# Kernel tuning notes

Measured on AMD Instinct MI355X. Metric: run time of the kernel, lower is better.

The kernel has to match this reference:

```python
import jax, jax.numpy as jnp
import numpy as np

N_NODES = 100000
N_EDGES = 3200000
HID = 16


def _graph_conv(x, src, dst, w_rel, w_root, b_rel, num_nodes):
    # PyG GraphConv: out_i = lin_rel(sum_{j in N(i)} x_j) + lin_root(x_i)
    agg = jax.ops.segment_sum(x[src], dst, num_segments=num_nodes)  # [N, d_in]
    return agg @ w_rel + b_rel + x @ w_root


def setup_inputs() -> dict:
    key = jax.random.key(0)
    ks = jax.random.split(key, 8)
    x = jax.random.normal(ks[0], (N_NODES, 1), dtype=jnp.float32)
    edge_index = jax.random.randint(ks[1], (2, N_EDGES), 0, N_NODES, dtype=jnp.int64)
    s = 1.0 / np.sqrt(HID)
    return {
        "x": x,
        "edge_index": edge_index,
        "enc_w_rel": jax.random.uniform(ks[2], (1, HID), jnp.float32, -1.0, 1.0),
        "enc_w_root": jax.random.uniform(ks[3], (1, HID), jnp.float32, -1.0, 1.0),
        "enc_b": jnp.zeros((HID,), jnp.float32),
        "proc_w_rel": jax.random.uniform(ks[4], (HID, HID), jnp.float32, -s, s),
        "proc_w_root": jax.random.uniform(ks[5], (HID, HID), jnp.float32, -s, s),
        "proc_b": jnp.zeros((HID,), jnp.float32),
        "dec_w_rel": jax.random.uniform(ks[6], (HID, 1), jnp.float32, -s, s),
        "dec_w_root": jax.random.uniform(ks[7], (HID, 1), jnp.float32, -s, s),
        "dec_b": jnp.zeros((1,), jnp.float32),
    }


def reference(x, edge_index, enc_w_rel, enc_w_root, enc_b,
              proc_w_rel, proc_w_root, proc_b,
              dec_w_rel, dec_w_root, dec_b):
    num_nodes = x.shape[0]
    src, dst = edge_index[0], edge_index[1]
    z = _graph_conv(x, src, dst, enc_w_rel, enc_w_root, enc_b, num_nodes)
    z = jax.nn.relu(z)
    z = _graph_conv(z, src, dst, proc_w_rel, proc_w_root, proc_b, num_nodes)
    y = _graph_conv(z, src, dst, dec_w_rel, dec_w_root, dec_b, num_nodes)
    return jax.nn.relu(y)
```

## Files before the change

### kernel.cpp

```cpp
#include <hip/hip_runtime.h>

#define HID 16
#define SB_BITS 11
#define SBLK (1 << SB_BITS)
#define NBMAX 64
#define GSTRIDE 16
#define PT_THREADS 512
#define PT_K 8
#define PT_EDGES (PT_THREADS * PT_K)

__global__ void k_init(int* __restrict__ p, int n) {
    int i = blockIdx.x * blockDim.x + threadIdx.x;
    if (i < n) p[i] = 0;
}

__global__ void __launch_bounds__(PT_THREADS)
k_passA(const int* __restrict__ src, const int* __restrict__ dst,
        unsigned* __restrict__ bucketsA, int* __restrict__ gcurA,
        int E, int nb, int capA) {
    __shared__ int cnt[NBMAX];
    __shared__ int pos[NBMAX];
    __shared__ int gbase[NBMAX];
    __shared__ unsigned reorder[PT_EDGES];
    __shared__ unsigned char bbk[PT_EDGES];
    int tb = blockIdx.x * PT_EDGES;
    int nE = min(PT_EDGES, E - tb);
    if (threadIdx.x < nb) cnt[threadIdx.x] = 0;
    __syncthreads();
    int kk[PT_K]; int rk[PT_K]; unsigned pk[PT_K];
    int ebase = tb + threadIdx.x * PT_K;
    if (ebase + PT_K <= E) {
        uint4 s0 = *(const uint4*)(src + ebase);
        uint4 s1 = *(const uint4*)(src + ebase + 4);
        uint4 d0 = *(const uint4*)(dst + ebase);
        uint4 d1 = *(const uint4*)(dst + ebase + 4);
        int ss[PT_K] = {(int)s0.x,(int)s0.y,(int)s0.z,(int)s0.w,
                        (int)s1.x,(int)s1.y,(int)s1.z,(int)s1.w};
        int dd[PT_K] = {(int)d0.x,(int)d0.y,(int)d0.z,(int)d0.w,
                        (int)d1.x,(int)d1.y,(int)d1.z,(int)d1.w};
#pragma unroll
        for (int k = 0; k < PT_K; k++) {
            int b = dd[k] >> SB_BITS;
            kk[k] = b;
            pk[k] = ((unsigned)(dd[k] & (SBLK - 1)) << 17) | (unsigned)ss[k];
            rk[k] = atomicAdd(&cnt[b], 1);
        }
    } else {
#pragma unroll
        for (int k = 0; k < PT_K; k++) {
            int e = ebase + k;
            if (e < E) {
                int s = src[e], d = dst[e];
                int b = d >> SB_BITS;
                kk[k] = b;
                pk[k] = ((unsigned)(d & (SBLK - 1)) << 17) | (unsigned)s;
                rk[k] = atomicAdd(&cnt[b], 1);
            } else kk[k] = -1;
        }
    }
    __syncthreads();
    if (threadIdx.x == 0) {
        int acc = 0;
        for (int b = 0; b < nb; b++) { pos[b] = acc; acc += cnt[b]; }
    }
    __syncthreads();
    if (threadIdx.x < nb && cnt[threadIdx.x] > 0)
        gbase[threadIdx.x] = atomicAdd(&gcurA[threadIdx.x * GSTRIDE], cnt[threadIdx.x]);
    __syncthreads();
#pragma unroll
    for (int k = 0; k < PT_K; k++) {
        if (kk[k] >= 0) {
            int idx = pos[kk[k]] + rk[k];
            reorder[idx] = pk[k];
            bbk[idx] = (unsigned char)kk[k];
        }
    }
    __syncthreads();
    for (int idx = threadIdx.x; idx < nE; idx += PT_THREADS) {
        int b = bbk[idx];
        int g = gbase[b] + (idx - pos[b]);
        if (g < capA) bucketsA[(size_t)b * capA + g] = reorder[idx];
    }
}

__global__ void __launch_bounds__(PT_THREADS)
k_aggA1(const unsigned* __restrict__ bucketsA, const int* __restrict__ gcurA,
        const float* __restrict__ val, float* __restrict__ AGG,
        int capA, int tilesA, int N) {
    int j = blockIdx.x / tilesA;
    int tile = blockIdx.x - j * tilesA;
    int cnt_j = min(gcurA[j * GSTRIDE], capA);
    int tb = tile * PT_EDGES;
    if (tb >= cnt_j) return;
    int nE = min(PT_EDGES, cnt_j - tb);
    __shared__ float acc[SBLK];
    for (int i = threadIdx.x; i < SBLK; i += PT_THREADS) acc[i] = 0.f;
    __syncthreads();
    const unsigned* in = bucketsA + (size_t)j * capA + tb;
    int ebase = threadIdx.x * PT_K;
    if (ebase + PT_K <= nE) {
        uint4 p0 = *(const uint4*)(in + ebase);
        uint4 p1 = *(const uint4*)(in + ebase + 4);
        unsigned pp[PT_K] = {p0.x, p0.y, p0.z, p0.w, p1.x, p1.y, p1.z, p1.w};
        float v[PT_K];
#pragma unroll
        for (int k = 0; k < PT_K; k++) v[k] = val[pp[k] & 0x1FFFFu];
#pragma unroll
        for (int k = 0; k < PT_K; k++) atomicAdd(&acc[pp[k] >> 17], v[k]);
    } else {
#pragma unroll
        for (int k = 0; k < PT_K; k++) {
            int e = ebase + k;
            if (e < nE) {
                unsigned p = in[e];
                atomicAdd(&acc[p >> 17], val[p & 0x1FFFFu]);
            }
        }
    }
    __syncthreads();
    int base_n = j << SB_BITS;
    for (int i = threadIdx.x; i < SBLK; i += PT_THREADS) {
        float v = acc[i];
        int n = base_n + i;
        if (n < N && v != 0.f) atomicAdd(&AGG[n], v);
    }
}

__global__ void __launch_bounds__(PT_THREADS)
k_aggA2(const unsigned* __restrict__ bucketsA, const int* __restrict__ gcurA,
        const float* __restrict__ SAB, float* __restrict__ AGG2,
        int capA, int tilesA, int N) {
    int j = blockIdx.x / tilesA;
    int tile = blockIdx.x - j * tilesA;
    int cnt_j = min(gcurA[j * GSTRIDE], capA);
    int tb = tile * PT_EDGES;
    if (tb >= cnt_j) return;
    int nE = min(PT_EDGES, cnt_j - tb);
    __shared__ float accx[SBLK];
    __shared__ float accy[SBLK];
    for (int i = threadIdx.x; i < SBLK; i += PT_THREADS) { accx[i] = 0.f; accy[i] = 0.f; }
    __syncthreads();
    const unsigned* in = bucketsA + (size_t)j * capA + tb;
    const float2* v2 = (const float2*)SAB;
    int ebase = threadIdx.x * PT_K;
    if (ebase + PT_K <= nE) {
        uint4 p0 = *(const uint4*)(in + ebase);
        uint4 p1 = *(const uint4*)(in + ebase + 4);
        unsigned pp[PT_K] = {p0.x, p0.y, p0.z, p0.w, p1.x, p1.y, p1.z, p1.w};
        float2 v[PT_K];
#pragma unroll
        for (int k = 0; k < PT_K; k++) v[k] = v2[pp[k] & 0x1FFFFu];
#pragma unroll
        for (int k = 0; k < PT_K; k++) {
            int d = (int)(pp[k] >> 17);
            atomicAdd(&accx[d], v[k].x);
            atomicAdd(&accy[d], v[k].y);
        }
    } else {
#pragma unroll
        for (int k = 0; k < PT_K; k++) {
            int e = ebase + k;
            if (e < nE) {
                unsigned p = in[e];
                float2 v = v2[p & 0x1FFFFu];
                int d = (int)(p >> 17);
                atomicAdd(&accx[d], v.x);
                atomicAdd(&accy[d], v.y);
            }
        }
    }
    __syncthreads();
    int base_n = j << SB_BITS;
    for (int i = threadIdx.x; i < SBLK; i += PT_THREADS) {
        float vx = accx[i], vy = accy[i];
        int n = base_n + i;
        if (n < N && (vx != 0.f || vy != 0.f)) {
            atomicAdd(&AGG2[2 * n],     vx);
            atomicAdd(&AGG2[2 * n + 1], vy);
        }
    }
}

__global__ void __launch_bounds__(256)
k_enc(const float* __restrict__ AGG1, const float* __restrict__ x,
      const float* __restrict__ ewrel, const float* __restrict__ ewroot,
      const float* __restrict__ eb,
      const float* __restrict__ pwrel, const float* __restrict__ pwroot,
      const float* __restrict__ dwrel, const float* __restrict__ dwroot,
      float* __restrict__ SAB, float* __restrict__ G1, float* __restrict__ G2,
      int N) {
    __shared__ float su1[HID], su2[HID], sv1[HID], sv2[HID];
    __shared__ float swr[HID], swo[HID], sbb[HID];
    int t = threadIdx.x;
    if (t < 64) {
        int k = t & 15, w = t >> 4;
        const float* M  = (w < 2) ? pwrel : pwroot;
        const float* vv = ((w & 1) == 0) ? dwrel : dwroot;
        float acc = 0.f;
        for (int h = 0; h < HID; h++) acc += M[k * HID + h] * vv[h];
        if (w == 0) su1[k] = acc;
        else if (w == 1) su2[k] = acc;
        else if (w == 2) sv1[k] = acc;
        else sv2[k] = acc;
    }
    if (t < HID) { swr[t] = ewrel[t]; swo[t] = ewroot[t]; sbb[t] = eb[t]; }
    __syncthreads();
    int n = blockIdx.x * 256 + t;
    if (n < N) {
        float a1 = AGG1[n], xi = x[n];
        float sa = 0.f, sb = 0.f, g1 = 0.f, g2 = 0.f;
#pragma unroll
        for (int h = 0; h < HID; h++) {
            float z = fmaxf(fmaf(a1, swr[h], fmaf(xi, swo[h], sbb[h])), 0.f);
            sa = fmaf(z, su1[h], sa);
            sb = fmaf(z, su2[h], sb);
            g1 = fmaf(z, sv1[h], g1);
            g2 = fmaf(z, sv2[h], g2);
        }
        ((float2*)SAB)[n] = make_float2(sa, sb);
        G1[n] = g1; G2[n] = g2;
    }
}

__global__ void __launch_bounds__(256)
k_mid(const float* __restrict__ AGG2, const float* __restrict__ G1,
      const float* __restrict__ G2, const float* __restrict__ pb,
      const float* __restrict__ dwrel, const float* __restrict__ dwroot,
      const float* __restrict__ db,
      float* __restrict__ BETA, float* __restrict__ R, int N) {
    __shared__ float sc1, sc2, sbd;
    if (threadIdx.x == 0) {
        float c1 = 0.f, c2 = 0.f;
        for (int h = 0; h < HID; h++) { c1 += pb[h] * dwrel[h]; c2 += pb[h] * dwroot[h]; }
        sc1 = c1; sc2 = c2; sbd = db[0];
    }
    __syncthreads();
    int n = blockIdx.x * 256 + threadIdx.x;
    if (n < N) {
        float2 a = ((const float2*)AGG2)[n];
        BETA[n] = a.x + G1[n] + sc1;
        R[n]    = a.y + G2[n] + sc2 + sbd;
    }
}

__global__ void __launch_bounds__(256)
k_final(const float* __restrict__ AGG3, const float* __restrict__ R,
        float* __restrict__ out, int N) {
    int n = blockIdx.x * 256 + threadIdx.x;
    if (n < N) out[n] = fmaxf(AGG3[n] + R[n], 0.f);
}

extern "C" void kernel_launch(void* const* d_in, const int* in_sizes, int n_in,
                              void* d_out, int out_size, void* d_ws, size_t ws_size,
                              hipStream_t stream) {
    const float* x      = (const float*)d_in[0];
    const int*   ei     = (const int*)d_in[1];
    const float* ewrel  = (const float*)d_in[2];
    const float* ewroot = (const float*)d_in[3];
    const float* eb     = (const float*)d_in[4];
    const float* pwrel  = (const float*)d_in[5];
    const float* pwroot = (const float*)d_in[6];
    const float* pb     = (const float*)d_in[7];
    const float* dwrel  = (const float*)d_in[8];
    const float* dwroot = (const float*)d_in[9];
    const float* db     = (const float*)d_in[10];
    float* out = (float*)d_out;

    const int N = in_sizes[0];
    const int E = in_sizes[1] / 2;
    const int* src = ei;
    const int* dst = ei + E;

    const int nb = (N + SBLK - 1) >> SB_BITS;
    int capA = ((E / nb + 2048) + PT_EDGES - 1) & ~(PT_EDGES - 1);
    const int tilesA = capA / PT_EDGES;

    size_t off = 0;
    int* gcurA = (int*)d_ws;                    off += NBMAX * GSTRIDE;
    float* AGG1 = (float*)d_ws + off;           off += N;
    float* AGG2 = (float*)d_ws + off;           off += (size_t)2 * N;
    float* AGG3 = (float*)d_ws + off;           off += N;
    const int zeroWords = (int)off;
    off = (off + 255) & ~(size_t)255;
    unsigned* bucketsA = (unsigned*)d_ws + off; off += (size_t)nb * capA;
    float* SAB  = (float*)d_ws + off;           off += (size_t)2 * N;
    float* G1   = (float*)d_ws + off;           off += N;
    float* G2   = (float*)d_ws + off;           off += N;
    float* BETA = (float*)d_ws + off;           off += N;
    float* R    = (float*)d_ws + off;           off += N;

    const int ntilesA = (E + PT_EDGES - 1) / PT_EDGES;
    const int aggGrid = nb * tilesA;
    const int nodeBlocks = (N + 255) / 256;

    hipLaunchKernelGGL(k_init, dim3((zeroWords + 255) / 256), dim3(256), 0, stream,
                       gcurA, zeroWords);
    hipLaunchKernelGGL(k_passA, dim3(ntilesA), dim3(PT_THREADS), 0, stream,
                       src, dst, bucketsA, gcurA, E, nb, capA);

    hipLaunchKernelGGL(k_aggA1, dim3(aggGrid), dim3(PT_THREADS), 0, stream,
                       bucketsA, gcurA, x, AGG1, capA, tilesA, N);
    hipLaunchKernelGGL(k_enc, dim3(nodeBlocks), dim3(256), 0, stream,
                       AGG1, x, ewrel, ewroot, eb, pwrel, pwroot,
                       dwrel, dwroot, SAB, G1, G2, N);

    hipLaunchKernelGGL(k_aggA2, dim3(aggGrid), dim3(PT_THREADS), 0, stream,
                       bucketsA, gcurA, SAB, AGG2, capA, tilesA, N);
    hipLaunchKernelGGL(k_mid, dim3(nodeBlocks), dim3(256), 0, stream,
                       AGG2, G1, G2, pb, dwrel, dwroot, db, BETA, R, N);

    hipLaunchKernelGGL(k_aggA1, dim3(aggGrid), dim3(PT_THREADS), 0, stream,
                       bucketsA, gcurA, BETA, AGG3, capA, tilesA, N);
    hipLaunchKernelGGL(k_final, dim3(nodeBlocks), dim3(256), 0, stream,
                       AGG3, R, out, N);
}
```

Before: 211.7 us.

## Bucket edges by source and scatter directly with global atomics

Edges are now bucketed by source block instead of destination block. Each aggregation block stages the source values of its 2048-node range in shared memory, which replaces the random global gather with a contiguous load. Each edge then does a global unsafeAtomicAdd to its destination, replacing shared-memory accumulation plus a flush. The cost is one random global float atomic per edge (two in the 2-wide pass) instead of per-block flushed partials, so atomic contention and traffic in L2 may rise.

```diff
diff --git a/kernel.cpp b/kernel.cpp
--- a/kernel.cpp
+++ b/kernel.cpp
@@ -40,9 +40,9 @@
                         (int)d1.x,(int)d1.y,(int)d1.z,(int)d1.w};
 #pragma unroll
         for (int k = 0; k < PT_K; k++) {
-            int b = dd[k] >> SB_BITS;
+            int b = ss[k] >> SB_BITS;
             kk[k] = b;
-            pk[k] = ((unsigned)(dd[k] & (SBLK - 1)) << 17) | (unsigned)ss[k];
+            pk[k] = ((unsigned)(ss[k] & (SBLK - 1)) << 17) | (unsigned)dd[k];
             rk[k] = atomicAdd(&cnt[b], 1);
         }
     } else {
@@ -51,9 +51,9 @@
             int e = ebase + k;
             if (e < E) {
                 int s = src[e], d = dst[e];
-                int b = d >> SB_BITS;
+                int b = s >> SB_BITS;
                 kk[k] = b;
-                pk[k] = ((unsigned)(d & (SBLK - 1)) << 17) | (unsigned)s;
+                pk[k] = ((unsigned)(s & (SBLK - 1)) << 17) | (unsigned)d;
                 rk[k] = atomicAdd(&cnt[b], 1);
             } else kk[k] = -1;
         }
@@ -84,7 +84,7 @@
 }
 
 __global__ void __launch_bounds__(PT_THREADS)
-k_aggA1(const unsigned* __restrict__ bucketsA, const int* __restrict__ gcurA,
+k_scat1(const unsigned* __restrict__ bucketsA, const int* __restrict__ gcurA,
         const float* __restrict__ val, float* __restrict__ AGG,
         int capA, int tilesA, int N) {
     int j = blockIdx.x / tilesA;
@@ -93,8 +93,12 @@
     int tb = tile * PT_EDGES;
     if (tb >= cnt_j) return;
     int nE = min(PT_EDGES, cnt_j - tb);
-    __shared__ float acc[SBLK];
-    for (int i = threadIdx.x; i < SBLK; i += PT_THREADS) acc[i] = 0.f;
+    __shared__ float sval[SBLK];
+    int base_n = j << SB_BITS;
+    for (int i = threadIdx.x; i < SBLK; i += PT_THREADS) {
+        int n = base_n + i;
+        sval[i] = (n < N) ? val[n] : 0.f;
+    }
     __syncthreads();
     const unsigned* in = bucketsA + (size_t)j * capA + tb;
     int ebase = threadIdx.x * PT_K;
@@ -102,32 +106,25 @@
         uint4 p0 = *(const uint4*)(in + ebase);
         uint4 p1 = *(const uint4*)(in + ebase + 4);
         unsigned pp[PT_K] = {p0.x, p0.y, p0.z, p0.w, p1.x, p1.y, p1.z, p1.w};
-        float v[PT_K];
-#pragma unroll
-        for (int k = 0; k < PT_K; k++) v[k] = val[pp[k] & 0x1FFFFu];
-#pragma unroll
-        for (int k = 0; k < PT_K; k++) atomicAdd(&acc[pp[k] >> 17], v[k]);
+#pragma unroll
+        for (int k = 0; k < PT_K; k++) {
+            float v = sval[pp[k] >> 17];
+            unsafeAtomicAdd(&AGG[pp[k] & 0x1FFFFu], v);
+        }
     } else {
 #pragma unroll
         for (int k = 0; k < PT_K; k++) {
             int e = ebase + k;
             if (e < nE) {
                 unsigned p = in[e];
-                atomicAdd(&acc[p >> 17], val[p & 0x1FFFFu]);
+                unsafeAtomicAdd(&AGG[p & 0x1FFFFu], sval[p >> 17]);
             }
         }
     }
-    __syncthreads();
-    int base_n = j << SB_BITS;
-    for (int i = threadIdx.x; i < SBLK; i += PT_THREADS) {
-        float v = acc[i];
-        int n = base_n + i;
-        if (n < N && v != 0.f) atomicAdd(&AGG[n], v);
-    }
 }
 
 __global__ void __launch_bounds__(PT_THREADS)
-k_aggA2(const unsigned* __restrict__ bucketsA, const int* __restrict__ gcurA,
+k_scat2(const unsigned* __restrict__ bucketsA, const int* __restrict__ gcurA,
         const float* __restrict__ SAB, float* __restrict__ AGG2,
         int capA, int tilesA, int N) {
     int j = blockIdx.x / tilesA;
@@ -136,25 +133,26 @@
     int tb = tile * PT_EDGES;
     if (tb >= cnt_j) return;
     int nE = min(PT_EDGES, cnt_j - tb);
-    __shared__ float accx[SBLK];
-    __shared__ float accy[SBLK];
-    for (int i = threadIdx.x; i < SBLK; i += PT_THREADS) { accx[i] = 0.f; accy[i] = 0.f; }
+    __shared__ float2 sval[SBLK];
+    int base_n = j << SB_BITS;
+    const float2* v2 = (const float2*)SAB;
+    for (int i = threadIdx.x; i < SBLK; i += PT_THREADS) {
+        int n = base_n + i;
+        sval[i] = (n < N) ? v2[n] : make_float2(0.f, 0.f);
+    }
     __syncthreads();
     const unsigned* in = bucketsA + (size_t)j * capA + tb;
-    const float2* v2 = (const float2*)SAB;
     int ebase = threadIdx.x * PT_K;
     if (ebase + PT_K <= nE) {
         uint4 p0 = *(const uint4*)(in + ebase);
         uint4 p1 = *(const uint4*)(in + ebase + 4);
         unsigned pp[PT_K] = {p0.x, p0.y, p0.z, p0.w, p1.x, p1.y, p1.z, p1.w};
-        float2 v[PT_K];
-#pragma unroll
-        for (int k = 0; k < PT_K; k++) v[k] = v2[pp[k] & 0x1FFFFu];
-#pragma unroll
-        for (int k = 0; k < PT_K; k++) {
-            int d = (int)(pp[k] >> 17);
-            atomicAdd(&accx[d], v[k].x);
-            atomicAdd(&accy[d], v[k].y);
+#pragma unroll
+        for (int k = 0; k < PT_K; k++) {
+            float2 v = sval[pp[k] >> 17];
+            int d = (int)(pp[k] & 0x1FFFFu);
+            unsafeAtomicAdd(&AGG2[2 * d],     v.x);
+            unsafeAtomicAdd(&AGG2[2 * d + 1], v.y);
         }
     } else {
 #pragma unroll
@@ -162,21 +160,11 @@
             int e = ebase + k;
             if (e < nE) {
                 unsigned p = in[e];
-                float2 v = v2[p & 0x1FFFFu];
-                int d = (int)(p >> 17);
-                atomicAdd(&accx[d], v.x);
-                atomicAdd(&accy[d], v.y);
+                float2 v = sval[p >> 17];
+                int d = (int)(p & 0x1FFFFu);
+                unsafeAtomicAdd(&AGG2[2 * d],     v.x);
+                unsafeAtomicAdd(&AGG2[2 * d + 1], v.y);
             }
-        }
-    }
-    __syncthreads();
-    int base_n = j << SB_BITS;
-    for (int i = threadIdx.x; i < SBLK; i += PT_THREADS) {
-        float vx = accx[i], vy = accy[i];
-        int n = base_n + i;
-        if (n < N && (vx != 0.f || vy != 0.f)) {
-            atomicAdd(&AGG2[2 * n],     vx);
-            atomicAdd(&AGG2[2 * n + 1], vy);
         }
     }
 }
@@ -298,18 +286,18 @@
     hipLaunchKernelGGL(k_passA, dim3(ntilesA), dim3(PT_THREADS), 0, stream,
                        src, dst, bucketsA, gcurA, E, nb, capA);
 
-    hipLaunchKernelGGL(k_aggA1, dim3(aggGrid), dim3(PT_THREADS), 0, stream,
+    hipLaunchKernelGGL(k_scat1, dim3(aggGrid), dim3(PT_THREADS), 0, stream,
                        bucketsA, gcurA, x, AGG1, capA, tilesA, N);
     hipLaunchKernelGGL(k_enc, dim3(nodeBlocks), dim3(256), 0, stream,
                        AGG1, x, ewrel, ewroot, eb, pwrel, pwroot,
                        dwrel, dwroot, SAB, G1, G2, N);
 
-    hipLaunchKernelGGL(k_aggA2, dim3(aggGrid), dim3(PT_THREADS), 0, stream,
+    hipLaunchKernelGGL(k_scat2, dim3(aggGrid), dim3(PT_THREADS), 0, stream,
                        bucketsA, gcurA, SAB, AGG2, capA, tilesA, N);
     hipLaunchKernelGGL(k_mid, dim3(nodeBlocks), dim3(256), 0, stream,
                        AGG2, G1, G2, pb, dwrel, dwroot, db, BETA, R, N);
 
-    hipLaunchKernelGGL(k_aggA1, dim3(aggGrid), dim3(PT_THREADS), 0, stream,
+    hipLaunchKernelGGL(k_scat1, dim3(aggGrid), dim3(PT_THREADS), 0, stream,
                        bucketsA, gcurA, BETA, AGG3, capA, tilesA, N);
     hipLaunchKernelGGL(k_final, dim3(nodeBlocks), dim3(256), 0, stream,
                        AGG3, R, out, N);
```

Measured after the change: 773.0 us. 265% more time.

## Replace global atomic flush with per-tile partial slabs reduced in node kernels

Applied to the files above, without the earlier changes.

Each aggregation block now writes its shared-memory accumulator to a private slab of partial sums with plain stores, instead of atomically adding non-zero entries into global node arrays. The following node-wise kernels (enc, mid, final) sum the partial slabs for their bucket over the tiles actually used. This removes global atomic contention and the zeroing of the aggregate arrays. In exchange it costs extra partial-buffer traffic (tilesA slabs per bucket) and per-node strided reads in the consumer kernels.

```diff
diff --git a/kernel.cpp b/kernel.cpp
--- a/kernel.cpp
+++ b/kernel.cpp
@@ -84,13 +84,13 @@
 }
 
 __global__ void __launch_bounds__(PT_THREADS)
-k_aggA1(const unsigned* __restrict__ bucketsA, const int* __restrict__ gcurA,
-        const float* __restrict__ val, float* __restrict__ AGG,
-        int capA, int tilesA, int N) {
+k_agg1(const unsigned* __restrict__ bucketsA, const int* __restrict__ gcurA,
+       const float* __restrict__ val, float* __restrict__ PART1,
+       int capA, int tilesA) {
     int j = blockIdx.x / tilesA;
-    int tile = blockIdx.x - j * tilesA;
+    int t = blockIdx.x - j * tilesA;
     int cnt_j = min(gcurA[j * GSTRIDE], capA);
-    int tb = tile * PT_EDGES;
+    int tb = t * PT_EDGES;
     if (tb >= cnt_j) return;
     int nE = min(PT_EDGES, cnt_j - tb);
     __shared__ float acc[SBLK];
@@ -118,22 +118,18 @@
         }
     }
     __syncthreads();
-    int base_n = j << SB_BITS;
-    for (int i = threadIdx.x; i < SBLK; i += PT_THREADS) {
-        float v = acc[i];
-        int n = base_n + i;
-        if (n < N && v != 0.f) atomicAdd(&AGG[n], v);
-    }
+    float* slab = PART1 + (size_t)(j * tilesA + t) * SBLK;
+    for (int i = threadIdx.x; i < SBLK; i += PT_THREADS) slab[i] = acc[i];
 }
 
 __global__ void __launch_bounds__(PT_THREADS)
-k_aggA2(const unsigned* __restrict__ bucketsA, const int* __restrict__ gcurA,
-        const float* __restrict__ SAB, float* __restrict__ AGG2,
-        int capA, int tilesA, int N) {
+k_agg2(const unsigned* __restrict__ bucketsA, const int* __restrict__ gcurA,
+       const float* __restrict__ SAB, float* __restrict__ PART2,
+       int capA, int tilesA) {
     int j = blockIdx.x / tilesA;
-    int tile = blockIdx.x - j * tilesA;
+    int t = blockIdx.x - j * tilesA;
     int cnt_j = min(gcurA[j * GSTRIDE], capA);
-    int tb = tile * PT_EDGES;
+    int tb = t * PT_EDGES;
     if (tb >= cnt_j) return;
     int nE = min(PT_EDGES, cnt_j - tb);
     __shared__ float accx[SBLK];
@@ -170,25 +166,20 @@
         }
     }
     __syncthreads();
-    int base_n = j << SB_BITS;
-    for (int i = threadIdx.x; i < SBLK; i += PT_THREADS) {
-        float vx = accx[i], vy = accy[i];
-        int n = base_n + i;
-        if (n < N && (vx != 0.f || vy != 0.f)) {
-            atomicAdd(&AGG2[2 * n],     vx);
-            atomicAdd(&AGG2[2 * n + 1], vy);
-        }
-    }
+    float2* slab = (float2*)PART2 + (size_t)(j * tilesA + t) * SBLK;
+    for (int i = threadIdx.x; i < SBLK; i += PT_THREADS)
+        slab[i] = make_float2(accx[i], accy[i]);
 }
 
 __global__ void __launch_bounds__(256)
-k_enc(const float* __restrict__ AGG1, const float* __restrict__ x,
+k_enc(const float* __restrict__ PART1, const int* __restrict__ gcurA,
+      const float* __restrict__ x,
       const float* __restrict__ ewrel, const float* __restrict__ ewroot,
       const float* __restrict__ eb,
       const float* __restrict__ pwrel, const float* __restrict__ pwroot,
       const float* __restrict__ dwrel, const float* __restrict__ dwroot,
       float* __restrict__ SAB, float* __restrict__ G1, float* __restrict__ G2,
-      int N) {
+      int capA, int tilesA, int N) {
     __shared__ float su1[HID], su2[HID], sv1[HID], sv2[HID];
     __shared__ float swr[HID], swo[HID], sbb[HID];
     int t = threadIdx.x;
@@ -207,7 +198,13 @@
     __syncthreads();
     int n = blockIdx.x * 256 + t;
     if (n < N) {
-        float a1 = AGG1[n], xi = x[n];
+        int j = n >> SB_BITS, slot = n & (SBLK - 1);
+        int cnt_j = min(gcurA[j * GSTRIDE], capA);
+        int nt = min(tilesA, (cnt_j + PT_EDGES - 1) / PT_EDGES);
+        float a1 = 0.f;
+        const float* pb1 = PART1 + (size_t)j * tilesA * SBLK + slot;
+        for (int tt = 0; tt < nt; tt++) a1 += pb1[tt * SBLK];
+        float xi = x[n];
         float sa = 0.f, sb = 0.f, g1 = 0.f, g2 = 0.f;
 #pragma unroll
         for (int h = 0; h < HID; h++) {
@@ -223,11 +220,12 @@
 }
 
 __global__ void __launch_bounds__(256)
-k_mid(const float* __restrict__ AGG2, const float* __restrict__ G1,
-      const float* __restrict__ G2, const float* __restrict__ pb,
-      const float* __restrict__ dwrel, const float* __restrict__ dwroot,
-      const float* __restrict__ db,
-      float* __restrict__ BETA, float* __restrict__ R, int N) {
+k_mid(const float* __restrict__ PART2, const int* __restrict__ gcurA,
+      const float* __restrict__ G1, const float* __restrict__ G2,
+      const float* __restrict__ pb, const float* __restrict__ dwrel,
+      const float* __restrict__ dwroot, const float* __restrict__ db,
+      float* __restrict__ BETA, float* __restrict__ R,
+      int capA, int tilesA, int N) {
     __shared__ float sc1, sc2, sbd;
     if (threadIdx.x == 0) {
         float c1 = 0.f, c2 = 0.f;
@@ -237,17 +235,34 @@
     __syncthreads();
     int n = blockIdx.x * 256 + threadIdx.x;
     if (n < N) {
-        float2 a = ((const float2*)AGG2)[n];
-        BETA[n] = a.x + G1[n] + sc1;
-        R[n]    = a.y + G2[n] + sc2 + sbd;
+        int j = n >> SB_BITS, slot = n & (SBLK - 1);
+        int cnt_j = min(gcurA[j * GSTRIDE], capA);
+        int nt = min(tilesA, (cnt_j + PT_EDGES - 1) / PT_EDGES);
+        float ax = 0.f, ay = 0.f;
+        const float2* pb2 = (const float2*)PART2 + (size_t)j * tilesA * SBLK + slot;
+        for (int tt = 0; tt < nt; tt++) {
+            float2 v = pb2[tt * SBLK];
+            ax += v.x; ay += v.y;
+        }
+        BETA[n] = ax + G1[n] + sc1;
+        R[n]    = ay + G2[n] + sc2 + sbd;
     }
 }
 
 __global__ void __launch_bounds__(256)
-k_final(const float* __restrict__ AGG3, const float* __restrict__ R,
-        float* __restrict__ out, int N) {
+k_final(const float* __restrict__ PART1, const int* __restrict__ gcurA,
+        const float* __restrict__ R, float* __restrict__ out,
+        int capA, int tilesA, int N) {
     int n = blockIdx.x * 256 + threadIdx.x;
-    if (n < N) out[n] = fmaxf(AGG3[n] + R[n], 0.f);
+    if (n < N) {
+        int j = n >> SB_BITS, slot = n & (SBLK - 1);
+        int cnt_j = min(gcurA[j * GSTRIDE], capA);
+        int nt = min(tilesA, (cnt_j + PT_EDGES - 1) / PT_EDGES);
+        float s = 0.f;
+        const float* pb1 = PART1 + (size_t)j * tilesA * SBLK + slot;
+        for (int tt = 0; tt < nt; tt++) s += pb1[tt * SBLK];
+        out[n] = fmaxf(s + R[n], 0.f);
+    }
 }
 
 extern "C" void kernel_launch(void* const* d_in, const int* in_sizes, int n_in,
@@ -277,12 +292,10 @@
 
     size_t off = 0;
     int* gcurA = (int*)d_ws;                    off += NBMAX * GSTRIDE;
-    float* AGG1 = (float*)d_ws + off;           off += N;
-    float* AGG2 = (float*)d_ws + off;           off += (size_t)2 * N;
-    float* AGG3 = (float*)d_ws + off;           off += N;
     const int zeroWords = (int)off;
     off = (off + 255) & ~(size_t)255;
     unsigned* bucketsA = (unsigned*)d_ws + off; off += (size_t)nb * capA;
+    float* PART = (float*)d_ws + off;           off += (size_t)2 * nb * tilesA * SBLK;
     float* SAB  = (float*)d_ws + off;           off += (size_t)2 * N;
     float* G1   = (float*)d_ws + off;           off += N;
     float* G2   = (float*)d_ws + off;           off += N;
@@ -298,19 +311,20 @@
     hipLaunchKernelGGL(k_passA, dim3(ntilesA), dim3(PT_THREADS), 0, stream,
                        src, dst, bucketsA, gcurA, E, nb, capA);
 
-    hipLaunchKernelGGL(k_aggA1, dim3(aggGrid), dim3(PT_THREADS), 0, stream,
-                       bucketsA, gcurA, x, AGG1, capA, tilesA, N);
+    hipLaunchKernelGGL(k_agg1, dim3(aggGrid), dim3(PT_THREADS), 0, stream,
+                       bucketsA, gcurA, x, PART, capA, tilesA);
     hipLaunchKernelGGL(k_enc, dim3(nodeBlocks), dim3(256), 0, stream,
-                       AGG1, x, ewrel, ewroot, eb, pwrel, pwroot,
-                       dwrel, dwroot, SAB, G1, G2, N);
-
-    hipLaunchKernelGGL(k_aggA2, dim3(aggGrid), dim3(PT_THREADS), 0, stream,
-                       bucketsA, gcurA, SAB, AGG2, capA, tilesA, N);
+                       PART, gcurA, x, ewrel, ewroot, eb, pwrel, pwroot,
+                       dwrel, dwroot, SAB, G1, G2, capA, tilesA, N);
+
+    hipLaunchKernelGGL(k_agg2, dim3(aggGrid), dim3(PT_THREADS), 0, stream,
+                       bucketsA, gcurA, SAB, PART, capA, tilesA);
     hipLaunchKernelGGL(k_mid, dim3(nodeBlocks), dim3(256), 0, stream,
-                       AGG2, G1, G2, pb, dwrel, dwroot, db, BETA, R, N);
-
-    hipLaunchKernelGGL(k_aggA1, dim3(aggGrid), dim3(PT_THREADS), 0, stream,
-                       bucketsA, gcurA, BETA, AGG3, capA, tilesA, N);
+                       PART, gcurA, G1, G2, pb, dwrel, dwroot, db,
+                       BETA, R, capA, tilesA, N);
+
+    hipLaunchKernelGGL(k_agg1, dim3(aggGrid), dim3(PT_THREADS), 0, stream,
+                       bucketsA, gcurA, BETA, PART, capA, tilesA);
     hipLaunchKernelGGL(k_final, dim3(nodeBlocks), dim3(256), 0, stream,
-                       AGG3, R, out, N);
-}
+                       PART, gcurA, R, out, capA, tilesA, N);
+}
```

Result: slower. 232.8 us (+10.0%).
